# Optimization experiments

Hardware: AMD Instinct MI355X
Metric: run time of the kernel (lower is better)

## Reference

```python
import jax, jax.numpy as jnp
import numpy as np
from jax import lax

B, N = 8, 4096
H = 128          # cfg.net.num_hidden
K = 64           # max_num_neighbors
R1, R2 = 0.2, 0.4
S1, S2 = N // 2, N // 8   # sampling ratios 0.5 and 0.25
OUT = 40


def setup_inputs() -> dict:
    key = jax.random.key(0)
    ks = jax.random.split(key, 32)
    inp = {}
    inp["x"] = jax.random.normal(ks[30], (B, N, 3), jnp.float32)
    inp["pos"] = jax.random.uniform(ks[31], (B, N, 3), jnp.float32)  # unit cube -> radii 0.2/0.4 meaningful
    layers = [("sa1_w1", "sa1_b1", 6, H // 2), ("sa1_w2", "sa1_b2", H // 2, H),
              ("sa2_w1", "sa2_b1", H + 3, H), ("sa2_w2", "sa2_b2", H, 2 * H),
              ("sa3_w1", "sa3_b1", 2 * H + 3, 2 * H), ("sa3_w2", "sa3_b2", 2 * H, 4 * H),
              ("sa3_w3", "sa3_b3", 4 * H, 8 * H),
              ("hd_w1", "hd_b1", 8 * H, 4 * H), ("hd_w2", "hd_b2", 4 * H, 2 * H),
              ("hd_w3", "hd_b3", 2 * H, OUT)]
    for i, (wn, bn, fi, fo) in enumerate(layers):
        inp[wn] = jax.random.normal(ks[i], (fi, fo), jnp.float32) / np.sqrt(fi)
        inp[bn] = jnp.zeros((fo,), jnp.float32)
    return inp


def _mlp(h, layers):
    # Linear+ReLU stack, plain last layer (PyG MLP plain_last=True, eval-mode BN is identity)
    n = len(layers)
    for i, (w, b) in enumerate(layers):
        h = h @ w + b
        if i < n - 1:
            h = jax.nn.relu(h)
    return h


def _fps(p, n_samples):
    # farthest point sampling on one cloud p: [N,3] -> [n_samples] int32
    Np = p.shape[0]

    def step(carry, _):
        min_d, last = carry
        d = jnp.sum((p - p[last]) ** 2, -1)
        min_d = jnp.minimum(min_d, d)
        return (min_d, jnp.argmax(min_d).astype(jnp.int32)), last

    _, idxs = lax.scan(step, (jnp.full((Np,), jnp.inf, p.dtype), jnp.int32(0)),
                       None, length=n_samples)
    return idxs


def _sa(xc, pc, n_samples, r, layers):
    # one SA layer on one cloud: xc [N,C], pc [N,3]
    idx = _fps(pc, n_samples)
    c = pc[idx]                                            # [S,3] centers
    d2 = jnp.sum((c[:, None, :] - pc[None, :, :]) ** 2, -1)  # [S,N]
    d2 = jnp.where(d2 <= r * r, d2, jnp.inf)               # ball query mask
    negd, nbr = lax.top_k(-d2, K)                          # K nearest inside ball
    valid = jnp.isfinite(negd)                             # [S,K]
    feat = jnp.concatenate([xc[nbr], pc[nbr] - c[:, None, :]], -1)  # [S,K,C+3]
    h = _mlp(feat, layers)                                 # [S,K,Cout]
    h = jnp.where(valid[..., None], h, -jnp.inf)
    return jnp.max(h, axis=1), c                           # max-pool over neighborhood


def reference(x, pos, sa1_w1, sa1_b1, sa1_w2, sa1_b2,
              sa2_w1, sa2_b1, sa2_w2, sa2_b2,
              sa3_w1, sa3_b1, sa3_w2, sa3_b2, sa3_w3, sa3_b3,
              hd_w1, hd_b1, hd_w2, hd_b2, hd_w3, hd_b3):
    x1, p1 = jax.vmap(lambda xc, pc: _sa(xc, pc, S1, R1,
                                         [(sa1_w1, sa1_b1), (sa1_w2, sa1_b2)]))(x, pos)
    x2, p2 = jax.vmap(lambda xc, pc: _sa(xc, pc, S2, R2,
                                         [(sa2_w1, sa2_b1), (sa2_w2, sa2_b2)]))(x1, p1)
    # GlobalSAModule: MLP(cat([x,pos])) then global max pool over remaining points
    g = _mlp(jnp.concatenate([x2, p2], -1),
             [(sa3_w1, sa3_b1), (sa3_w2, sa3_b2), (sa3_w3, sa3_b3)])
    g = jnp.max(g, axis=1)                                 # [B, 8H]
    # head MLP (dropout inactive at eval)
    return _mlp(g, [(hd_w1, hd_b1), (hd_w2, hd_b2), (hd_w3, hd_b3)])
```

## Files before the change

kernel.cpp:

```cpp
#include <hip/hip_runtime.h>


constexpr int NBATCH = 8;

template<int CTRL>
__device__ __forceinline__ float dpp_max_step(float v) {
  int o = __builtin_amdgcn_update_dpp(__float_as_int(v), __float_as_int(v),
                                      CTRL, 0xf, 0xf, false);
  return fmaxf(v, __int_as_float(o));
}
__device__ __forceinline__ float wave_max_bcast(float v) {
  v = dpp_max_step<0x111>(v);
  v = dpp_max_step<0x112>(v);
  v = dpp_max_step<0x114>(v);
  v = dpp_max_step<0x118>(v);
  v = dpp_max_step<0x142>(v);
  v = dpp_max_step<0x143>(v);
  return __int_as_float(__builtin_amdgcn_readlane(__float_as_int(v), 63));
}
template<int CTRL>
__device__ __forceinline__ int dpp_add_step(int v) {
  int o = __builtin_amdgcn_update_dpp(0, v, CTRL, 0xf, 0xf, true);
  return v + o;
}
__device__ __forceinline__ int wave_sum_bcast(int v) {
  v = dpp_add_step<0x111>(v);
  v = dpp_add_step<0x112>(v);
  v = dpp_add_step<0x114>(v);
  v = dpp_add_step<0x118>(v);
  v = dpp_add_step<0x142>(v);
  v = dpp_add_step<0x143>(v);
  return __builtin_amdgcn_readlane(v, 63);
}

template<int NPTS, int NTH, int NSAMP>
__device__ void fps_body(const float* __restrict__ p, float* __restrict__ cb) {
#pragma clang fp contract(off)
  constexpr int PT = NPTS / NTH;
  constexpr int NW = NTH / 64;
  __shared__ float lx[NPTS], ly[NPTS], lz[NPTS];
  __shared__ unsigned long long wkey[2][NW];
  __shared__ int sidx[NSAMP];
  const int t = threadIdx.x, lane = t & 63, w = t >> 6;
  float px[PT], py[PT], pz[PT], md[PT];
#pragma unroll
  for (int i = 0; i < PT; i++) {
    int j = t * PT + i;
    px[i] = p[j * 3 + 0]; py[i] = p[j * 3 + 1]; pz[i] = p[j * 3 + 2];
    lx[j] = px[i]; ly[j] = py[i]; lz[j] = pz[i];
    md[i] = __builtin_inff();
  }
  __syncthreads();
  int cur = 0;
  for (int s = 0;; ++s) {
    float cx = lx[cur], cy = ly[cur], cz = lz[cur];
    if (t == 0) sidx[s] = cur;
    if (s == NSAMP - 1) break;
    float bv = -__builtin_inff(); int bi = 0;
#pragma unroll
    for (int i = 0; i < PT; i++) {
      float dx = px[i] - cx, dy = py[i] - cy, dz = pz[i] - cz;
      float d = (dx * dx + dy * dy) + dz * dz;
      float m = fminf(md[i], d); md[i] = m;
      if (m > bv) { bv = m; bi = i; }
    }
    float wmax = wave_max_bcast(bv);
    unsigned long long ball = __ballot(bv == wmax);
    int fl = __ffsll((long long)ball) - 1;
    int ib = __builtin_amdgcn_readlane(bi, fl);
    int gidx = ((w << 6) + fl) * PT + ib;
    if (lane == 0)
      wkey[s & 1][w] = (((unsigned long long)(unsigned)__float_as_int(wmax)) << 32)
                       | (unsigned)(~gidx);
    __syncthreads();
    unsigned long long best = wkey[s & 1][0];
#pragma unroll
    for (int q = 1; q < NW; q++) {
      unsigned long long k2 = wkey[s & 1][q];
      if (k2 > best) best = k2;
    }
    cur = (int)(~(unsigned)best);
  }
  __syncthreads();
  for (int i = t; i < NSAMP; i += NTH) {
    int id = sidx[i];
    cb[i * 3 + 0] = lx[id]; cb[i * 3 + 1] = ly[id]; cb[i * 3 + 2] = lz[id];
  }
}

template<int NPTS, int SPB>
__device__ void ballquery_body(int bb, const float* __restrict__ pts,
    const float* __restrict__ ctr, float rr,
    int* __restrict__ nbr, int* __restrict__ cnt_out) {
#pragma clang fp contract(off)
  const int gw = (bb << 2) + (threadIdx.x >> 6);
  const int lane = threadIdx.x & 63;
  const int b = gw / SPB;
  __shared__ unsigned long long list_[4][1024];
  unsigned long long* list = list_[threadIdx.x >> 6];
  const float* p = pts + (size_t)b * NPTS * 3;
  const float* c = ctr + (size_t)gw * 3;
  const float cx = c[0], cy = c[1], cz = c[2];
  const unsigned long long lmask = (1ull << lane) - 1ull;
  int cnt = 0;
  for (int j0 = 0; j0 < NPTS; j0 += 64) {
    int j = j0 + lane;
    float dx = p[j * 3 + 0] - cx, dy = p[j * 3 + 1] - cy, dz = p[j * 3 + 2] - cz;
    float d = (dx * dx + dy * dy) + dz * dz;
    bool in = (d <= rr);
    unsigned long long bal = __ballot(in);
    int pos = cnt + __popcll(bal & lmask);
    if (in && pos < 1024)
      list[pos] = (((unsigned long long)__float_as_uint(d)) << 32) | (unsigned)j;
    cnt += __popcll(bal);
  }
  if (cnt > 1024) cnt = 1024;
  __syncthreads();
  int* nbrp = nbr + (size_t)gw * 64;
  const int nr = (cnt + 63) >> 6;
  unsigned long long key[16];
#pragma unroll
  for (int r = 0; r < 16; r++) {
    int slot = r * 64 + lane;
    key[r] = (r < nr && slot < cnt) ? list[slot] : ~0ull;
  }
  if (cnt <= 64) {
    nbrp[lane] = (lane < cnt) ? (int)(unsigned)key[0] : 0;
    if (lane == 0) cnt_out[gw] = cnt;
    return;
  }
  unsigned pref = 0; int cbase = 0;
  for (int bit = 29; bit >= 0; --bit) {
    int cc = 0;
#pragma unroll
    for (int r = 0; r < 16; r++) if (r < nr) {
      unsigned db = (unsigned)(key[r] >> 32);
      cc += ((db >> bit) == (pref >> bit)) ? 1 : 0;
    }
    cc = wave_sum_bcast(cc);
    if (cbase + cc < 64) { cbase += cc; pref |= (1u << bit); }
  }
  int base = 0;
#pragma unroll
  for (int r = 0; r < 16; r++) if (r < nr) {
    unsigned db = (unsigned)(key[r] >> 32);
    bool sel = db < pref;
    unsigned long long m = __ballot(sel);
    if (sel) nbrp[base + __popcll(m & lmask)] = (int)(unsigned)key[r];
    base += __popcll(m);
  }
  int need = 64 - base;
  for (int t2 = 0; t2 < need; ++t2) {
    unsigned besti = 0xffffffffu;
#pragma unroll
    for (int r = 0; r < 16; r++) if (r < nr) {
      if ((unsigned)(key[r] >> 32) == pref) {
        unsigned v = (unsigned)key[r];
        besti = v < besti ? v : besti;
      }
    }
#pragma unroll
    for (int off = 32; off; off >>= 1) {
      unsigned o = __shfl_xor(besti, off, 64);
      besti = o < besti ? o : besti;
    }
    unsigned long long wk = (((unsigned long long)pref) << 32) | besti;
#pragma unroll
    for (int r = 0; r < 16; r++) if (r < nr && key[r] == wk) key[r] = ~0ull;
    if (lane == 0) nbrp[base + t2] = (int)besti;
  }
  if (lane == 0) cnt_out[gw] = 64;
}

__device__ void q1_body(int bb, const float* __restrict__ x,
    const float* __restrict__ pos, const float* __restrict__ w, float* __restrict__ q) {
  int gw = bb * 8 + (threadIdx.x >> 6), lane = threadIdx.x & 63;
  const float* xr = x + (size_t)gw * 3; const float* pr = pos + (size_t)gw * 3;
  float a = 0.f;
#pragma unroll
  for (int m = 0; m < 3; m++) a = fmaf(xr[m], w[m * 64 + lane], a);
#pragma unroll
  for (int m = 0; m < 3; m++) a = fmaf(pr[m], w[(3 + m) * 64 + lane], a);
  q[(size_t)gw * 64 + lane] = a;
}

__device__ void t1_body(int bb, const float* __restrict__ c1,
    const float* __restrict__ w, const float* __restrict__ b1, float* __restrict__ t) {
  int gw = (bb << 2) + (threadIdx.x >> 6), lane = threadIdx.x & 63;
  const float* cr = c1 + (size_t)gw * 3;
  float a = b1[lane];
#pragma unroll
  for (int m = 0; m < 3; m++) a = fmaf(-cr[m], w[(3 + m) * 64 + lane], a);
  t[(size_t)gw * 64 + lane] = a;
}

__device__ void t2_body(int bb, const float* __restrict__ c2,
    const float* __restrict__ w, const float* __restrict__ b1, float* __restrict__ t) {
  int gw = (bb << 2) + (threadIdx.x >> 6), lane = threadIdx.x & 63;
  const float* cr = c2 + (size_t)gw * 3;
  float a0 = b1[lane], a1 = b1[64 + lane];
#pragma unroll
  for (int m = 0; m < 3; m++) {
    a0 = fmaf(-cr[m], w[(128 + m) * 128 + lane], a0);
    a1 = fmaf(-cr[m], w[(128 + m) * 128 + 64 + lane], a1);
  }
  t[(size_t)gw * 128 + lane] = a0;
  t[(size_t)gw * 128 + 64 + lane] = a1;
}

__device__ void concat3_body(int bb, const float* __restrict__ c2, float* __restrict__ xin3) {
  int row = bb * 256 + threadIdx.x;
  if (row < NBATCH * 512) {
    float* o = xin3 + (size_t)row * 272 + 256;
    const float* c = c2 + (size_t)row * 3;
    o[0] = c[0]; o[1] = c[1]; o[2] = c[2];
#pragma unroll
    for (int i = 3; i < 16; i++) o[i] = 0.f;
  }
}

template<int CIN, int COUT, int OSTR, int NPB, int SPB>
__device__ void sa_pool_body(int bb, const float* __restrict__ q,
    const float* __restrict__ t, const int* __restrict__ nbr, const int* __restrict__ cnt,
    const float* __restrict__ w2, const float* __restrict__ b2, float* __restrict__ out) {
  int gw = (bb << 2) + (threadIdx.x >> 6), lane = threadIdx.x & 63;
  int b = gw / SPB;
  int nk = nbr[(size_t)gw * 64 + lane];
  int c = cnt[gw];
  const float* qr = q + ((size_t)b * NPB + nk) * CIN;
  const float* tr = t + (size_t)gw * CIN;
  float h[CIN];
#pragma unroll
  for (int i = 0; i < CIN; i += 4) {
    float4 v = *(const float4*)(qr + i);
    h[i]     = fmaxf(v.x + tr[i], 0.f);
    h[i + 1] = fmaxf(v.y + tr[i + 1], 0.f);
    h[i + 2] = fmaxf(v.z + tr[i + 2], 0.f);
    h[i + 3] = fmaxf(v.w + tr[i + 3], 0.f);
  }
  bool valid = lane < c;
  float* op = out + (size_t)gw * OSTR;
#pragma unroll 1
  for (int nc = 0; nc < COUT; nc += 16) {
    float acc[16];
#pragma unroll
    for (int u = 0; u < 16; u++) acc[u] = b2[nc + u];
#pragma unroll
    for (int i = 0; i < CIN; i++) {
      const float* wr = w2 + (size_t)i * COUT + nc;
#pragma unroll
      for (int u = 0; u < 16; u++) acc[u] = fmaf(h[i], wr[u], acc[u]);
    }
#pragma unroll
    for (int u = 0; u < 16; u++) {
      float v = valid ? acc[u] : -__builtin_inff();
#pragma unroll
      for (int off = 32; off; off >>= 1) v = fmaxf(v, __shfl_xor(v, off, 64));
      acc[u] = v;
    }
    if (lane == 0) {
#pragma unroll
      for (int u = 0; u < 16; u += 4)
        *(float4*)(op + nc + u) = make_float4(acc[u], acc[u + 1], acc[u + 2], acc[u + 3]);
    }
  }
}

__global__ __launch_bounds__(512) void fuse1_kernel(const float* __restrict__ pos,
    const float* __restrict__ x, const float* __restrict__ w11,
    float* __restrict__ c1, float* __restrict__ q1) {
  int bid = blockIdx.x;
  if (bid < 8)
    fps_body<4096, 512, 2048>(pos + (size_t)bid * 4096 * 3, c1 + (size_t)bid * 2048 * 3);
  else
    q1_body(bid - 8, x, pos, w11, q1);
}

__global__ __launch_bounds__(256) void fuse2_kernel(const float* __restrict__ pos,
    const float* __restrict__ c1, const float* __restrict__ w11, const float* __restrict__ b11,
    float* __restrict__ c2, int* __restrict__ nbr1, int* __restrict__ cnt1,
    float* __restrict__ t1buf, float rr1) {
  int bid = blockIdx.x;
  if (bid < 8)
    fps_body<2048, 256, 512>(c1 + (size_t)bid * 2048 * 3, c2 + (size_t)bid * 512 * 3);
  else if (bid < 8 + 4096)
    ballquery_body<4096, 2048>(bid - 8, pos, c1, rr1, nbr1, cnt1);
  else
    t1_body(bid - (8 + 4096), c1, w11, b11, t1buf);
}

__global__ __launch_bounds__(256) void fuse3_kernel(const float* __restrict__ q1buf,
    const float* __restrict__ t1buf, const int* __restrict__ nbr1, const int* __restrict__ cnt1,
    const float* __restrict__ w12, const float* __restrict__ b12, float* __restrict__ x1,
    const float* __restrict__ c1, const float* __restrict__ c2, float rr2,
    int* __restrict__ nbr2, int* __restrict__ cnt2,
    const float* __restrict__ w21, const float* __restrict__ b21, float* __restrict__ t2buf,
    float* __restrict__ xin3) {
  int bid = blockIdx.x;
  if (bid < 4096)
    sa_pool_body<64, 128, 128, 4096, 2048>(bid, q1buf, t1buf, nbr1, cnt1, w12, b12, x1);
  else if (bid < 4096 + 1024)
    ballquery_body<2048, 512>(bid - 4096, c1, c2, rr2, nbr2, cnt2);
  else if (bid < 4096 + 1024 + 1024)
    t2_body(bid - (4096 + 1024), c2, w21, b21, t2buf);
  else
    concat3_body(bid - (4096 + 1024 + 1024), c2, xin3);
}

__global__ __launch_bounds__(256) void q2_kernel(const float* __restrict__ x1,
    const float* __restrict__ p1, const float* __restrict__ w, float* __restrict__ q2) {
  int gw = (blockIdx.x << 2) + (threadIdx.x >> 6), lane = threadIdx.x & 63;
  const float* xr = x1 + (size_t)gw * 128; const float* pr = p1 + (size_t)gw * 3;
  float a0 = 0.f, a1 = 0.f;
#pragma unroll 8
  for (int m = 0; m < 128; m++) {
    float v = xr[m];
    a0 = fmaf(v, w[m * 128 + lane], a0);
    a1 = fmaf(v, w[m * 128 + 64 + lane], a1);
  }
#pragma unroll
  for (int m = 0; m < 3; m++) {
    float v = pr[m];
    a0 = fmaf(v, w[(128 + m) * 128 + lane], a0);
    a1 = fmaf(v, w[(128 + m) * 128 + 64 + lane], a1);
  }
  q2[(size_t)gw * 128 + lane] = a0;
  q2[(size_t)gw * 128 + 64 + lane] = a1;
}

__global__ __launch_bounds__(256) void sa_pool2_kernel(const float* __restrict__ q,
    const float* __restrict__ t, const int* __restrict__ nbr, const int* __restrict__ cnt,
    const float* __restrict__ w2, const float* __restrict__ b2, float* __restrict__ out) {
  sa_pool_body<128, 256, 272, 2048, 512>(blockIdx.x, q, t, nbr, cnt, w2, b2, out);
}

template<int K, int KP, int N, int AST, bool RELU>
__global__ __launch_bounds__(256) void gemm64(const float* __restrict__ A,
    const float* __restrict__ W, const float* __restrict__ bias, float* __restrict__ C) {
  constexpr int NT = N / 64;
  const int bid = blockIdx.x, tid = threadIdx.x;
  const int tm = bid / NT, tn = bid % NT;
  __shared__ __align__(16) float As[16][68];
  __shared__ __align__(16) float Ws[16][68];
  const int arow = tid >> 2, acol = (tid & 3) << 2;
  const int wrow = tid >> 4, wcol = (tid & 15) << 2;
  const int ty = tid >> 4, tx = tid & 15;
  const float* Ap = A + (size_t)(tm * 64 + arow) * AST + acol;
  const float* Wp = W + (size_t)tn * 64 + wcol;
  float acc[4][4] = {};
  for (int k0 = 0; k0 < KP; k0 += 16) {
    float4 av = *(const float4*)(Ap + k0);
    As[acol + 0][arow] = av.x; As[acol + 1][arow] = av.y;
    As[acol + 2][arow] = av.z; As[acol + 3][arow] = av.w;
    int krow = k0 + wrow;
    float4 wv = make_float4(0.f, 0.f, 0.f, 0.f);
    if (krow < K) wv = *(const float4*)(Wp + (size_t)krow * N);
    *(float4*)(&Ws[wrow][wcol]) = wv;
    __syncthreads();
#pragma unroll
    for (int kk = 0; kk < 16; kk++) {
      float4 a4 = *(const float4*)(&As[kk][ty << 2]);
      float4 b4 = *(const float4*)(&Ws[kk][tx << 2]);
      float aa[4] = {a4.x, a4.y, a4.z, a4.w};
      float bb[4] = {b4.x, b4.y, b4.z, b4.w};
#pragma unroll
      for (int mm = 0; mm < 4; mm++)
#pragma unroll
        for (int nn = 0; nn < 4; nn++) acc[mm][nn] = fmaf(aa[mm], bb[nn], acc[mm][nn]);
    }
    __syncthreads();
  }
  const int m0 = tm * 64 + (ty << 2), n0 = tn * 64 + (tx << 2);
#pragma unroll
  for (int mm = 0; mm < 4; mm++) {
    float4 o;
    o.x = acc[mm][0] + bias[n0 + 0];
    o.y = acc[mm][1] + bias[n0 + 1];
    o.z = acc[mm][2] + bias[n0 + 2];
    o.w = acc[mm][3] + bias[n0 + 3];
    if (RELU) { o.x = fmaxf(o.x, 0.f); o.y = fmaxf(o.y, 0.f);
                o.z = fmaxf(o.z, 0.f); o.w = fmaxf(o.w, 0.f); }
    *(float4*)(C + (size_t)(m0 + mm) * N + n0) = o;
  }
}

__global__ void gmax_kernel(const float* __restrict__ h, float* __restrict__ g) {
  int n = blockIdx.x * 256 + threadIdx.x;
  int b = n >> 10, col = n & 1023;
  const float* p = h + ((size_t)b * 512) * 1024 + col;
  float m = -__builtin_inff();
  for (int j = 0; j < 512; j++) m = fmaxf(m, p[(size_t)j * 1024]);
  g[n] = m;
}

__global__ __launch_bounds__(256) void head_kernel(const float* __restrict__ g,
    const float* __restrict__ w1, const float* __restrict__ b1,
    const float* __restrict__ w2, const float* __restrict__ b2,
    const float* __restrict__ w3, const float* __restrict__ b3,
    float* __restrict__ out) {
  int b = blockIdx.x, t = threadIdx.x;
  __shared__ float s1[1024];
  __shared__ float s2[512];
  *(float4*)(s1 + t * 4) = *(const float4*)(g + (size_t)b * 1024 + t * 4);
  __syncthreads();
  {
    float a0 = b1[t], a1 = b1[t + 256];
    for (int i = 0; i < 1024; i++) {
      float v = s1[i];
      a0 = fmaf(v, w1[(size_t)i * 512 + t], a0);
      a1 = fmaf(v, w1[(size_t)i * 512 + t + 256], a1);
    }
    s2[t] = fmaxf(a0, 0.f); s2[t + 256] = fmaxf(a1, 0.f);
  }
  __syncthreads();
  {
    float a = b2[t];
    for (int i = 0; i < 512; i++) a = fmaf(s2[i], w2[(size_t)i * 256 + t], a);
    s1[t] = fmaxf(a, 0.f);
  }
  __syncthreads();
  if (t < 40) {
    float a = b3[t];
    for (int i = 0; i < 256; i++) a = fmaf(s1[i], w3[(size_t)i * 40 + t], a);
    out[(size_t)b * 40 + t] = a;
  }
}

extern "C" void kernel_launch(void* const* d_in, const int* in_sizes, int n_in,
                              void* d_out, int out_size, void* d_ws, size_t ws_size,
                              hipStream_t stream) {
  const float* x   = (const float*)d_in[0];
  const float* pos = (const float*)d_in[1];
  const float* w11 = (const float*)d_in[2];  const float* b11 = (const float*)d_in[3];
  const float* w12 = (const float*)d_in[4];  const float* b12 = (const float*)d_in[5];
  const float* w21 = (const float*)d_in[6];  const float* b21 = (const float*)d_in[7];
  const float* w22 = (const float*)d_in[8];  const float* b22 = (const float*)d_in[9];
  const float* w31 = (const float*)d_in[10]; const float* b31 = (const float*)d_in[11];
  const float* w32 = (const float*)d_in[12]; const float* b32 = (const float*)d_in[13];
  const float* w33 = (const float*)d_in[14]; const float* b33 = (const float*)d_in[15];
  const float* hw1 = (const float*)d_in[16]; const float* hb1 = (const float*)d_in[17];
  const float* hw2 = (const float*)d_in[18]; const float* hb2 = (const float*)d_in[19];
  const float* hw3 = (const float*)d_in[20]; const float* hb3 = (const float*)d_in[21];
  float* out = (float*)d_out;

  char* wsb = (char*)d_ws;
  int*   cnt1 = (int*)(wsb + 81920);
  int*   cnt2 = (int*)(wsb + 147456);
  float* c1   = (float*)(wsb + 163840);
  float* c2   = (float*)(wsb + 360448);
  float* g    = (float*)(wsb + 409600);
  char* big = wsb + 524288;
  int*   nbr1 = (int*)(big + 0);
  float* q1   = (float*)(big + 4194304);
  float* t1   = (float*)(big + 12582912);
  float* h3c  = (float*)(big + 0);
  float* x1   = (float*)(big + 16777216);
  int*   nbr2 = (int*)(big + 25165824);
  float* h3b  = (float*)(big + 16777216);
  float* q2   = (float*)(big + 26214400);
  float* h3a  = (float*)(big + 26214400);
  float* t2   = (float*)(big + 34603008);
  float* xin3 = (float*)(big + 36700160);

  const float RR1 = (float)(0.2 * 0.2);
  const float RR2 = (float)(0.4 * 0.4);

  fuse1_kernel<<<8 + 4096, 512, 0, stream>>>(pos, x, w11, c1, q1);
  fuse2_kernel<<<8 + 4096 + 4096, 256, 0, stream>>>(pos, c1, w11, b11,
                                                    c2, nbr1, cnt1, t1, RR1);
  fuse3_kernel<<<4096 + 1024 + 1024 + 16, 256, 0, stream>>>(q1, t1, nbr1, cnt1,
      w12, b12, x1, c1, c2, RR2, nbr2, cnt2, w21, b21, t2, xin3);
  q2_kernel<<<4096, 256, 0, stream>>>(x1, c1, w21, q2);
  sa_pool2_kernel<<<1024, 256, 0, stream>>>(q2, t2, nbr2, cnt2, w22, b22, xin3);
  gemm64<259, 272, 256, 272, true ><<<256,  256, 0, stream>>>(xin3, w31, b31, h3a);
  gemm64<256, 256, 512, 256, true ><<<512,  256, 0, stream>>>(h3a,  w32, b32, h3b);
  gemm64<512, 512, 1024, 512, false><<<1024, 256, 0, stream>>>(h3b, w33, b33, h3c);
  gmax_kernel<<<32, 256, 0, stream>>>(h3c, g);
  head_kernel<<<NBATCH, 256, 0, stream>>>(g, hw1, hb1, hw2, hb2, hw3, hb3, out);

  (void)in_sizes; (void)n_in; (void)out_size; (void)ws_size;
}
```

Measured before the change: 3.535 ms.

## Interleave four clouds per FPS block with packed math and register-carried centers

Result: slower. 8.536 ms (+141.5%).

```diff
diff --git a/kernel.cpp b/kernel.cpp
--- a/kernel.cpp
+++ b/kernel.cpp
@@ -2,6 +2,8 @@
 
 
 constexpr int NBATCH = 8;
+
+typedef float v2f __attribute__((ext_vector_type(2)));
 
 template<int CTRL>
 __device__ __forceinline__ float dpp_max_step(float v) {
@@ -33,70 +35,215 @@
   return __builtin_amdgcn_readlane(v, 63);
 }
 
-template<int NPTS, int NTH, int NSAMP>
-__device__ void fps_body(const float* __restrict__ p, float* __restrict__ cb) {
+#define DIST_PAIR(PX, PY, PZ, MD) { \
+  v2f dx = PX - cxv; v2f dy = PY - cyv; v2f dz = PZ - czv; \
+  v2f d = (dx * dx + dy * dy) + dz * dz; \
+  MD = __builtin_elementwise_min(MD, d); \
+  bv2 = __builtin_elementwise_max(bv2, MD); }
+
+__device__ void fps1_quad(const float* __restrict__ pos4, float* __restrict__ cb4) {
 #pragma clang fp contract(off)
-  constexpr int PT = NPTS / NTH;
-  constexpr int NW = NTH / 64;
-  __shared__ float lx[NPTS], ly[NPTS], lz[NPTS];
-  __shared__ unsigned long long wkey[2][NW];
-  __shared__ int sidx[NSAMP];
+  constexpr int NPTS = 4096, NTH = 512, PT = 8, NW = 8, NSAMP = 2048;
+  __shared__ unsigned long long skey[2][4][NW];
+  __shared__ float sxyz[2][4][NW][3];
+  __shared__ float scb[4][NSAMP * 3];
   const int t = threadIdx.x, lane = t & 63, w = t >> 6;
-  float px[PT], py[PT], pz[PT], md[PT];
-#pragma unroll
-  for (int i = 0; i < PT; i++) {
-    int j = t * PT + i;
-    px[i] = p[j * 3 + 0]; py[i] = p[j * 3 + 1]; pz[i] = p[j * 3 + 2];
-    lx[j] = px[i]; ly[j] = py[i]; lz[j] = pz[i];
-    md[i] = __builtin_inff();
+  const float INF = __builtin_inff();
+
+#define F1_REGS(B) \
+  v2f px0_##B, px1_##B, px2_##B, px3_##B; \
+  v2f py0_##B, py1_##B, py2_##B, py3_##B; \
+  v2f pz0_##B, pz1_##B, pz2_##B, pz3_##B; \
+  v2f md0_##B, md1_##B, md2_##B, md3_##B; \
+  float cx_##B, cy_##B, cz_##B;
+  F1_REGS(0) F1_REGS(1) F1_REGS(2) F1_REGS(3)
+
+#define F1_LOAD(B) { \
+  const float* pp = pos4 + (size_t)(B) * NPTS * 3; \
+  int jb = t * PT; \
+  px0_##B = (v2f){pp[(jb+0)*3+0], pp[(jb+1)*3+0]}; \
+  py0_##B = (v2f){pp[(jb+0)*3+1], pp[(jb+1)*3+1]}; \
+  pz0_##B = (v2f){pp[(jb+0)*3+2], pp[(jb+1)*3+2]}; \
+  px1_##B = (v2f){pp[(jb+2)*3+0], pp[(jb+3)*3+0]}; \
+  py1_##B = (v2f){pp[(jb+2)*3+1], pp[(jb+3)*3+1]}; \
+  pz1_##B = (v2f){pp[(jb+2)*3+2], pp[(jb+3)*3+2]}; \
+  px2_##B = (v2f){pp[(jb+4)*3+0], pp[(jb+5)*3+0]}; \
+  py2_##B = (v2f){pp[(jb+4)*3+1], pp[(jb+5)*3+1]}; \
+  pz2_##B = (v2f){pp[(jb+4)*3+2], pp[(jb+5)*3+2]}; \
+  px3_##B = (v2f){pp[(jb+6)*3+0], pp[(jb+7)*3+0]}; \
+  py3_##B = (v2f){pp[(jb+6)*3+1], pp[(jb+7)*3+1]}; \
+  pz3_##B = (v2f){pp[(jb+6)*3+2], pp[(jb+7)*3+2]}; \
+  md0_##B = (v2f){INF, INF}; md1_##B = (v2f){INF, INF}; \
+  md2_##B = (v2f){INF, INF}; md3_##B = (v2f){INF, INF}; \
+  cx_##B = pp[0]; cy_##B = pp[1]; cz_##B = pp[2]; \
+  if (t == 0) { scb[B][0] = cx_##B; scb[B][1] = cy_##B; scb[B][2] = cz_##B; } }
+  F1_LOAD(0) F1_LOAD(1) F1_LOAD(2) F1_LOAD(3)
+
+#define F1_PHASEA(B) { \
+  v2f cxv = {cx_##B, cx_##B}, cyv = {cy_##B, cy_##B}, czv = {cz_##B, cz_##B}; \
+  v2f bv2 = (v2f){-INF, -INF}; \
+  DIST_PAIR(px0_##B, py0_##B, pz0_##B, md0_##B) \
+  DIST_PAIR(px1_##B, py1_##B, pz1_##B, md1_##B) \
+  DIST_PAIR(px2_##B, py2_##B, pz2_##B, md2_##B) \
+  DIST_PAIR(px3_##B, py3_##B, pz3_##B, md3_##B) \
+  float bv = fmaxf(bv2.x, bv2.y); \
+  int bi = 0; \
+  if (md3_##B.y == bv) bi = 7; \
+  if (md3_##B.x == bv) bi = 6; \
+  if (md2_##B.y == bv) bi = 5; \
+  if (md2_##B.x == bv) bi = 4; \
+  if (md1_##B.y == bv) bi = 3; \
+  if (md1_##B.x == bv) bi = 2; \
+  if (md0_##B.y == bv) bi = 1; \
+  if (md0_##B.x == bv) bi = 0; \
+  float wmax = wave_max_bcast(bv); \
+  unsigned long long ball = __ballot(bv == wmax); \
+  int fl = __ffsll((long long)ball) - 1; \
+  int ib = __builtin_amdgcn_readlane(bi, fl); \
+  int gidx = ((w << 6) + fl) * PT + ib; \
+  int kk = ib >> 1; \
+  v2f sx = px0_##B, sy = py0_##B, sz = pz0_##B; \
+  if (kk == 1) { sx = px1_##B; sy = py1_##B; sz = pz1_##B; } \
+  if (kk == 2) { sx = px2_##B; sy = py2_##B; sz = pz2_##B; } \
+  if (kk == 3) { sx = px3_##B; sy = py3_##B; sz = pz3_##B; } \
+  float wx = (ib & 1) ? sx.y : sx.x; \
+  float wy = (ib & 1) ? sy.y : sy.x; \
+  float wz = (ib & 1) ? sz.y : sz.x; \
+  wx = __int_as_float(__builtin_amdgcn_readlane(__float_as_int(wx), fl)); \
+  wy = __int_as_float(__builtin_amdgcn_readlane(__float_as_int(wy), fl)); \
+  wz = __int_as_float(__builtin_amdgcn_readlane(__float_as_int(wz), fl)); \
+  if (lane == 0) { \
+    skey[s & 1][B][w] = (((unsigned long long)(unsigned)__float_as_int(wmax)) << 32) \
+                        | (unsigned)(~gidx); \
+    sxyz[s & 1][B][w][0] = wx; sxyz[s & 1][B][w][1] = wy; sxyz[s & 1][B][w][2] = wz; } }
+
+#define F1_PHASEB(B) { \
+  unsigned long long best = skey[s & 1][B][0]; int qw = 0; \
+  _Pragma("unroll") \
+  for (int q = 1; q < NW; q++) { \
+    unsigned long long k2 = skey[s & 1][B][q]; \
+    if (k2 > best) { best = k2; qw = q; } } \
+  cx_##B = sxyz[s & 1][B][qw][0]; \
+  cy_##B = sxyz[s & 1][B][qw][1]; \
+  cz_##B = sxyz[s & 1][B][qw][2]; \
+  if (t == 0) { scb[B][(s + 1) * 3 + 0] = cx_##B; \
+                scb[B][(s + 1) * 3 + 1] = cy_##B; \
+                scb[B][(s + 1) * 3 + 2] = cz_##B; } }
+
+  for (int s = 0; s < NSAMP - 1; ++s) {
+    F1_PHASEA(0) F1_PHASEA(1) F1_PHASEA(2) F1_PHASEA(3)
+    __syncthreads();
+    F1_PHASEB(0) F1_PHASEB(1) F1_PHASEB(2) F1_PHASEB(3)
   }
   __syncthreads();
-  int cur = 0;
-  for (int s = 0;; ++s) {
-    float cx = lx[cur], cy = ly[cur], cz = lz[cur];
-    if (t == 0) sidx[s] = cur;
-    if (s == NSAMP - 1) break;
-    float bv = -__builtin_inff(); int bi = 0;
-#pragma unroll
-    for (int i = 0; i < PT; i++) {
-      float dx = px[i] - cx, dy = py[i] - cy, dz = pz[i] - cz;
-      float d = (dx * dx + dy * dy) + dz * dz;
-      float m = fminf(md[i], d); md[i] = m;
-      if (m > bv) { bv = m; bi = i; }
-    }
-    float wmax = wave_max_bcast(bv);
-    unsigned long long ball = __ballot(bv == wmax);
-    int fl = __ffsll((long long)ball) - 1;
-    int ib = __builtin_amdgcn_readlane(bi, fl);
-    int gidx = ((w << 6) + fl) * PT + ib;
-    if (lane == 0)
-      wkey[s & 1][w] = (((unsigned long long)(unsigned)__float_as_int(wmax)) << 32)
-                       | (unsigned)(~gidx);
+#pragma unroll
+  for (int B = 0; B < 4; B++)
+    for (int i = t; i < NSAMP * 3; i += NTH)
+      cb4[(size_t)B * NSAMP * 3 + i] = scb[B][i];
+#undef F1_REGS
+#undef F1_LOAD
+#undef F1_PHASEA
+#undef F1_PHASEB
+}
+
+__device__ void fps2_quad(const float* __restrict__ pos4, float* __restrict__ cb4) {
+#pragma clang fp contract(off)
+  constexpr int NPTS = 2048, NTH = 512, PT = 4, NW = 8, NSAMP = 512;
+  __shared__ unsigned long long skey2[2][4][NW];
+  __shared__ float sxyz2[2][4][NW][3];
+  __shared__ float scb2[4][NSAMP * 3];
+  const int t = threadIdx.x, lane = t & 63, w = t >> 6;
+  const float INF = __builtin_inff();
+
+#define F2_REGS(B) \
+  v2f px0_##B, px1_##B, py0_##B, py1_##B, pz0_##B, pz1_##B; \
+  v2f md0_##B, md1_##B; \
+  float cx_##B, cy_##B, cz_##B;
+  F2_REGS(0) F2_REGS(1) F2_REGS(2) F2_REGS(3)
+
+#define F2_LOAD(B) { \
+  const float* pp = pos4 + (size_t)(B) * NPTS * 3; \
+  int jb = t * PT; \
+  px0_##B = (v2f){pp[(jb+0)*3+0], pp[(jb+1)*3+0]}; \
+  py0_##B = (v2f){pp[(jb+0)*3+1], pp[(jb+1)*3+1]}; \
+  pz0_##B = (v2f){pp[(jb+0)*3+2], pp[(jb+1)*3+2]}; \
+  px1_##B = (v2f){pp[(jb+2)*3+0], pp[(jb+3)*3+0]}; \
+  py1_##B = (v2f){pp[(jb+2)*3+1], pp[(jb+3)*3+1]}; \
+  pz1_##B = (v2f){pp[(jb+2)*3+2], pp[(jb+3)*3+2]}; \
+  md0_##B = (v2f){INF, INF}; md1_##B = (v2f){INF, INF}; \
+  cx_##B = pp[0]; cy_##B = pp[1]; cz_##B = pp[2]; \
+  if (t == 0) { scb2[B][0] = cx_##B; scb2[B][1] = cy_##B; scb2[B][2] = cz_##B; } }
+  F2_LOAD(0) F2_LOAD(1) F2_LOAD(2) F2_LOAD(3)
+
+#define F2_PHASEA(B) { \
+  v2f cxv = {cx_##B, cx_##B}, cyv = {cy_##B, cy_##B}, czv = {cz_##B, cz_##B}; \
+  v2f bv2 = (v2f){-INF, -INF}; \
+  DIST_PAIR(px0_##B, py0_##B, pz0_##B, md0_##B) \
+  DIST_PAIR(px1_##B, py1_##B, pz1_##B, md1_##B) \
+  float bv = fmaxf(bv2.x, bv2.y); \
+  int bi = 0; \
+  if (md1_##B.y == bv) bi = 3; \
+  if (md1_##B.x == bv) bi = 2; \
+  if (md0_##B.y == bv) bi = 1; \
+  if (md0_##B.x == bv) bi = 0; \
+  float wmax = wave_max_bcast(bv); \
+  unsigned long long ball = __ballot(bv == wmax); \
+  int fl = __ffsll((long long)ball) - 1; \
+  int ib = __builtin_amdgcn_readlane(bi, fl); \
+  int gidx = ((w << 6) + fl) * PT + ib; \
+  int kk = ib >> 1; \
+  v2f sx = px0_##B, sy = py0_##B, sz = pz0_##B; \
+  if (kk == 1) { sx = px1_##B; sy = py1_##B; sz = pz1_##B; } \
+  float wx = (ib & 1) ? sx.y : sx.x; \
+  float wy = (ib & 1) ? sy.y : sy.x; \
+  float wz = (ib & 1) ? sz.y : sz.x; \
+  wx = __int_as_float(__builtin_amdgcn_readlane(__float_as_int(wx), fl)); \
+  wy = __int_as_float(__builtin_amdgcn_readlane(__float_as_int(wy), fl)); \
+  wz = __int_as_float(__builtin_amdgcn_readlane(__float_as_int(wz), fl)); \
+  if (lane == 0) { \
+    skey2[s & 1][B][w] = (((unsigned long long)(unsigned)__float_as_int(wmax)) << 32) \
+                         | (unsigned)(~gidx); \
+    sxyz2[s & 1][B][w][0] = wx; sxyz2[s & 1][B][w][1] = wy; sxyz2[s & 1][B][w][2] = wz; } }
+
+#define F2_PHASEB(B) { \
+  unsigned long long best = skey2[s & 1][B][0]; int qw = 0; \
+  _Pragma("unroll") \
+  for (int q = 1; q < NW; q++) { \
+    unsigned long long k2 = skey2[s & 1][B][q]; \
+    if (k2 > best) { best = k2; qw = q; } } \
+  cx_##B = sxyz2[s & 1][B][qw][0]; \
+  cy_##B = sxyz2[s & 1][B][qw][1]; \
+  cz_##B = sxyz2[s & 1][B][qw][2]; \
+  if (t == 0) { scb2[B][(s + 1) * 3 + 0] = cx_##B; \
+                scb2[B][(s + 1) * 3 + 1] = cy_##B; \
+                scb2[B][(s + 1) * 3 + 2] = cz_##B; } }
+
+  for (int s = 0; s < NSAMP - 1; ++s) {
+    F2_PHASEA(0) F2_PHASEA(1) F2_PHASEA(2) F2_PHASEA(3)
     __syncthreads();
-    unsigned long long best = wkey[s & 1][0];
-#pragma unroll
-    for (int q = 1; q < NW; q++) {
-      unsigned long long k2 = wkey[s & 1][q];
-      if (k2 > best) best = k2;
-    }
-    cur = (int)(~(unsigned)best);
+    F2_PHASEB(0) F2_PHASEB(1) F2_PHASEB(2) F2_PHASEB(3)
   }
   __syncthreads();
-  for (int i = t; i < NSAMP; i += NTH) {
-    int id = sidx[i];
-    cb[i * 3 + 0] = lx[id]; cb[i * 3 + 1] = ly[id]; cb[i * 3 + 2] = lz[id];
-  }
-}
-
-template<int NPTS, int SPB>
+#pragma unroll
+  for (int B = 0; B < 4; B++)
+    for (int i = t; i < NSAMP * 3; i += NTH)
+      cb4[(size_t)B * NSAMP * 3 + i] = scb2[B][i];
+#undef F2_REGS
+#undef F2_LOAD
+#undef F2_PHASEA
+#undef F2_PHASEB
+}
+
+template<int NPTS, int SPB, int LCAP, int WPB>
 __device__ void ballquery_body(int bb, const float* __restrict__ pts,
     const float* __restrict__ ctr, float rr,
     int* __restrict__ nbr, int* __restrict__ cnt_out) {
 #pragma clang fp contract(off)
-  const int gw = (bb << 2) + (threadIdx.x >> 6);
+  constexpr int KREG = LCAP / 64;
+  const int gw = bb * WPB + (threadIdx.x >> 6);
   const int lane = threadIdx.x & 63;
   const int b = gw / SPB;
-  __shared__ unsigned long long list_[4][1024];
+  __shared__ unsigned long long list_[WPB][LCAP];
   unsigned long long* list = list_[threadIdx.x >> 6];
   const float* p = pts + (size_t)b * NPTS * 3;
   const float* c = ctr + (size_t)gw * 3;
@@ -110,17 +257,17 @@
     bool in = (d <= rr);
     unsigned long long bal = __ballot(in);
     int pos = cnt + __popcll(bal & lmask);
-    if (in && pos < 1024)
+    if (in && pos < LCAP)
       list[pos] = (((unsigned long long)__float_as_uint(d)) << 32) | (unsigned)j;
     cnt += __popcll(bal);
   }
-  if (cnt > 1024) cnt = 1024;
+  if (cnt > LCAP) cnt = LCAP;
   __syncthreads();
   int* nbrp = nbr + (size_t)gw * 64;
   const int nr = (cnt + 63) >> 6;
-  unsigned long long key[16];
-#pragma unroll
-  for (int r = 0; r < 16; r++) {
+  unsigned long long key[KREG];
+#pragma unroll
+  for (int r = 0; r < KREG; r++) {
     int slot = r * 64 + lane;
     key[r] = (r < nr && slot < cnt) ? list[slot] : ~0ull;
   }
@@ -133,7 +280,7 @@
   for (int bit = 29; bit >= 0; --bit) {
     int cc = 0;
 #pragma unroll
-    for (int r = 0; r < 16; r++) if (r < nr) {
+    for (int r = 0; r < KREG; r++) if (r < nr) {
       unsigned db = (unsigned)(key[r] >> 32);
       cc += ((db >> bit) == (pref >> bit)) ? 1 : 0;
     }
@@ -142,7 +289,7 @@
   }
   int base = 0;
 #pragma unroll
-  for (int r = 0; r < 16; r++) if (r < nr) {
+  for (int r = 0; r < KREG; r++) if (r < nr) {
     unsigned db = (unsigned)(key[r] >> 32);
     bool sel = db < pref;
     unsigned long long m = __ballot(sel);
@@ -153,7 +300,7 @@
   for (int t2 = 0; t2 < need; ++t2) {
     unsigned besti = 0xffffffffu;
 #pragma unroll
-    for (int r = 0; r < 16; r++) if (r < nr) {
+    for (int r = 0; r < KREG; r++) if (r < nr) {
       if ((unsigned)(key[r] >> 32) == pref) {
         unsigned v = (unsigned)key[r];
         besti = v < besti ? v : besti;
@@ -166,7 +313,7 @@
     }
     unsigned long long wk = (((unsigned long long)pref) << 32) | besti;
 #pragma unroll
-    for (int r = 0; r < 16; r++) if (r < nr && key[r] == wk) key[r] = ~0ull;
+    for (int r = 0; r < KREG; r++) if (r < nr && key[r] == wk) key[r] = ~0ull;
     if (lane == 0) nbrp[base + t2] = (int)besti;
   }
   if (lane == 0) cnt_out[gw] = 64;
@@ -186,7 +333,7 @@
 
 __device__ void t1_body(int bb, const float* __restrict__ c1,
     const float* __restrict__ w, const float* __restrict__ b1, float* __restrict__ t) {
-  int gw = (bb << 2) + (threadIdx.x >> 6), lane = threadIdx.x & 63;
+  int gw = bb * 8 + (threadIdx.x >> 6), lane = threadIdx.x & 63;
   const float* cr = c1 + (size_t)gw * 3;
   float a = b1[lane];
 #pragma unroll
@@ -270,23 +417,23 @@
     const float* __restrict__ x, const float* __restrict__ w11,
     float* __restrict__ c1, float* __restrict__ q1) {
   int bid = blockIdx.x;
-  if (bid < 8)
-    fps_body<4096, 512, 2048>(pos + (size_t)bid * 4096 * 3, c1 + (size_t)bid * 2048 * 3);
+  if (bid < 2)
+    fps1_quad(pos + (size_t)bid * 4 * 4096 * 3, c1 + (size_t)bid * 4 * 2048 * 3);
   else
-    q1_body(bid - 8, x, pos, w11, q1);
-}
-
-__global__ __launch_bounds__(256) void fuse2_kernel(const float* __restrict__ pos,
+    q1_body(bid - 2, x, pos, w11, q1);
+}
+
+__global__ __launch_bounds__(512) void fuse2_kernel(const float* __restrict__ pos,
     const float* __restrict__ c1, const float* __restrict__ w11, const float* __restrict__ b11,
     float* __restrict__ c2, int* __restrict__ nbr1, int* __restrict__ cnt1,
     float* __restrict__ t1buf, float rr1) {
   int bid = blockIdx.x;
-  if (bid < 8)
-    fps_body<2048, 256, 512>(c1 + (size_t)bid * 2048 * 3, c2 + (size_t)bid * 512 * 3);
-  else if (bid < 8 + 4096)
-    ballquery_body<4096, 2048>(bid - 8, pos, c1, rr1, nbr1, cnt1);
+  if (bid < 2)
+    fps2_quad(c1 + (size_t)bid * 4 * 2048 * 3, c2 + (size_t)bid * 4 * 512 * 3);
+  else if (bid < 2 + 2048)
+    ballquery_body<4096, 2048, 512, 8>(bid - 2, pos, c1, rr1, nbr1, cnt1);
   else
-    t1_body(bid - (8 + 4096), c1, w11, b11, t1buf);
+    t1_body(bid - (2 + 2048), c1, w11, b11, t1buf);
 }
 
 __global__ __launch_bounds__(256) void fuse3_kernel(const float* __restrict__ q1buf,
@@ -300,7 +447,7 @@
   if (bid < 4096)
     sa_pool_body<64, 128, 128, 4096, 2048>(bid, q1buf, t1buf, nbr1, cnt1, w12, b12, x1);
   else if (bid < 4096 + 1024)
-    ballquery_body<2048, 512>(bid - 4096, c1, c2, rr2, nbr2, cnt2);
+    ballquery_body<2048, 512, 1024, 4>(bid - 4096, c1, c2, rr2, nbr2, cnt2);
   else if (bid < 4096 + 1024 + 1024)
     t2_body(bid - (4096 + 1024), c2, w21, b21, t2buf);
   else
@@ -465,8 +612,8 @@
   const float RR1 = (float)(0.2 * 0.2);
   const float RR2 = (float)(0.4 * 0.4);
 
-  fuse1_kernel<<<8 + 4096, 512, 0, stream>>>(pos, x, w11, c1, q1);
-  fuse2_kernel<<<8 + 4096 + 4096, 256, 0, stream>>>(pos, c1, w11, b11,
+  fuse1_kernel<<<2 + 4096, 512, 0, stream>>>(pos, x, w11, c1, q1);
+  fuse2_kernel<<<2 + 2048 + 2048, 512, 0, stream>>>(pos, c1, w11, b11,
                                                     c2, nbr1, cnt1, t1, RR1);
   fuse3_kernel<<<4096 + 1024 + 1024 + 16, 256, 0, stream>>>(q1, t1, nbr1, cnt1,
       w12, b12, x1, c1, c2, RR2, nbr2, cnt2, w21, b21, t2, xin3);
```

## Vectorize FPS with packed float2 math and carry winner coordinates through reduction

Applied to the files above, without the earlier changes.

Measured after the change: 4.116 ms. 1.16x slower.

```diff
diff --git a/kernel.cpp b/kernel.cpp
--- a/kernel.cpp
+++ b/kernel.cpp
@@ -2,6 +2,8 @@
 
 
 constexpr int NBATCH = 8;
+
+typedef float v2f __attribute__((ext_vector_type(2)));
 
 template<int CTRL>
 __device__ __forceinline__ float dpp_max_step(float v) {
@@ -33,70 +35,180 @@
   return __builtin_amdgcn_readlane(v, 63);
 }
 
-template<int NPTS, int NTH, int NSAMP>
-__device__ void fps_body(const float* __restrict__ p, float* __restrict__ cb) {
+#define DIST_PAIR(PX, PY, PZ, MD) { \
+  v2f dx = PX - cxv; v2f dy = PY - cyv; v2f dz = PZ - czv; \
+  v2f d = (dx * dx + dy * dy) + dz * dz; \
+  MD = __builtin_elementwise_min(MD, d); \
+  bv2 = __builtin_elementwise_max(bv2, MD); }
+
+__device__ void fps1_one(const float* __restrict__ p, float* __restrict__ cb) {
 #pragma clang fp contract(off)
-  constexpr int PT = NPTS / NTH;
-  constexpr int NW = NTH / 64;
-  __shared__ float lx[NPTS], ly[NPTS], lz[NPTS];
-  __shared__ unsigned long long wkey[2][NW];
-  __shared__ int sidx[NSAMP];
+  constexpr int NTH = 512, PT = 8, NW = 8, NSAMP = 2048;
+  __shared__ unsigned long long skey[2][NW];
+  __shared__ float sxyz[2][NW][3];
+  __shared__ float scb[NSAMP * 3];
   const int t = threadIdx.x, lane = t & 63, w = t >> 6;
-  float px[PT], py[PT], pz[PT], md[PT];
-#pragma unroll
-  for (int i = 0; i < PT; i++) {
-    int j = t * PT + i;
-    px[i] = p[j * 3 + 0]; py[i] = p[j * 3 + 1]; pz[i] = p[j * 3 + 2];
-    lx[j] = px[i]; ly[j] = py[i]; lz[j] = pz[i];
-    md[i] = __builtin_inff();
-  }
-  __syncthreads();
-  int cur = 0;
-  for (int s = 0;; ++s) {
-    float cx = lx[cur], cy = ly[cur], cz = lz[cur];
-    if (t == 0) sidx[s] = cur;
-    if (s == NSAMP - 1) break;
-    float bv = -__builtin_inff(); int bi = 0;
-#pragma unroll
-    for (int i = 0; i < PT; i++) {
-      float dx = px[i] - cx, dy = py[i] - cy, dz = pz[i] - cz;
-      float d = (dx * dx + dy * dy) + dz * dz;
-      float m = fminf(md[i], d); md[i] = m;
-      if (m > bv) { bv = m; bi = i; }
-    }
+  const float INF = __builtin_inff();
+  v2f px0, px1, px2, px3, py0, py1, py2, py3, pz0, pz1, pz2, pz3;
+  v2f md0, md1, md2, md3;
+  {
+    int jb = t * PT;
+    px0 = (v2f){p[(jb+0)*3+0], p[(jb+1)*3+0]};
+    py0 = (v2f){p[(jb+0)*3+1], p[(jb+1)*3+1]};
+    pz0 = (v2f){p[(jb+0)*3+2], p[(jb+1)*3+2]};
+    px1 = (v2f){p[(jb+2)*3+0], p[(jb+3)*3+0]};
+    py1 = (v2f){p[(jb+2)*3+1], p[(jb+3)*3+1]};
+    pz1 = (v2f){p[(jb+2)*3+2], p[(jb+3)*3+2]};
+    px2 = (v2f){p[(jb+4)*3+0], p[(jb+5)*3+0]};
+    py2 = (v2f){p[(jb+4)*3+1], p[(jb+5)*3+1]};
+    pz2 = (v2f){p[(jb+4)*3+2], p[(jb+5)*3+2]};
+    px3 = (v2f){p[(jb+6)*3+0], p[(jb+7)*3+0]};
+    py3 = (v2f){p[(jb+6)*3+1], p[(jb+7)*3+1]};
+    pz3 = (v2f){p[(jb+6)*3+2], p[(jb+7)*3+2]};
+    md0 = (v2f){INF, INF}; md1 = (v2f){INF, INF};
+    md2 = (v2f){INF, INF}; md3 = (v2f){INF, INF};
+  }
+  float cx = p[0], cy = p[1], cz = p[2];
+  if (t == 0) { scb[0] = cx; scb[1] = cy; scb[2] = cz; }
+  for (int s = 0; s < NSAMP - 1; ++s) {
+    v2f cxv = {cx, cx}, cyv = {cy, cy}, czv = {cz, cz};
+    v2f bv2 = (v2f){-INF, -INF};
+    DIST_PAIR(px0, py0, pz0, md0)
+    DIST_PAIR(px1, py1, pz1, md1)
+    DIST_PAIR(px2, py2, pz2, md2)
+    DIST_PAIR(px3, py3, pz3, md3)
+    float bv = fmaxf(bv2.x, bv2.y);
+    int bi = 0;
+    if (md3.y == bv) bi = 7;
+    if (md3.x == bv) bi = 6;
+    if (md2.y == bv) bi = 5;
+    if (md2.x == bv) bi = 4;
+    if (md1.y == bv) bi = 3;
+    if (md1.x == bv) bi = 2;
+    if (md0.y == bv) bi = 1;
+    if (md0.x == bv) bi = 0;
     float wmax = wave_max_bcast(bv);
     unsigned long long ball = __ballot(bv == wmax);
     int fl = __ffsll((long long)ball) - 1;
     int ib = __builtin_amdgcn_readlane(bi, fl);
     int gidx = ((w << 6) + fl) * PT + ib;
-    if (lane == 0)
-      wkey[s & 1][w] = (((unsigned long long)(unsigned)__float_as_int(wmax)) << 32)
+    int kk = ib >> 1;
+    v2f sx = px0, sy = py0, sz = pz0;
+    if (kk == 1) { sx = px1; sy = py1; sz = pz1; }
+    if (kk == 2) { sx = px2; sy = py2; sz = pz2; }
+    if (kk == 3) { sx = px3; sy = py3; sz = pz3; }
+    float wx = (ib & 1) ? sx.y : sx.x;
+    float wy = (ib & 1) ? sy.y : sy.x;
+    float wz = (ib & 1) ? sz.y : sz.x;
+    wx = __int_as_float(__builtin_amdgcn_readlane(__float_as_int(wx), fl));
+    wy = __int_as_float(__builtin_amdgcn_readlane(__float_as_int(wy), fl));
+    wz = __int_as_float(__builtin_amdgcn_readlane(__float_as_int(wz), fl));
+    if (lane == 0) {
+      skey[s & 1][w] = (((unsigned long long)(unsigned)__float_as_int(wmax)) << 32)
                        | (unsigned)(~gidx);
+      sxyz[s & 1][w][0] = wx; sxyz[s & 1][w][1] = wy; sxyz[s & 1][w][2] = wz;
+    }
     __syncthreads();
-    unsigned long long best = wkey[s & 1][0];
+    unsigned long long best = skey[s & 1][0];
+    float nx = sxyz[s & 1][0][0], ny = sxyz[s & 1][0][1], nz = sxyz[s & 1][0][2];
 #pragma unroll
     for (int q = 1; q < NW; q++) {
-      unsigned long long k2 = wkey[s & 1][q];
-      if (k2 > best) best = k2;
-    }
-    cur = (int)(~(unsigned)best);
+      unsigned long long k2 = skey[s & 1][q];
+      bool gt = k2 > best;
+      best = gt ? k2 : best;
+      nx = gt ? sxyz[s & 1][q][0] : nx;
+      ny = gt ? sxyz[s & 1][q][1] : ny;
+      nz = gt ? sxyz[s & 1][q][2] : nz;
+    }
+    cx = nx; cy = ny; cz = nz;
+    if (t == 0) { scb[(s + 1) * 3 + 0] = cx; scb[(s + 1) * 3 + 1] = cy;
+                  scb[(s + 1) * 3 + 2] = cz; }
   }
   __syncthreads();
-  for (int i = t; i < NSAMP; i += NTH) {
-    int id = sidx[i];
-    cb[i * 3 + 0] = lx[id]; cb[i * 3 + 1] = ly[id]; cb[i * 3 + 2] = lz[id];
-  }
-}
-
-template<int NPTS, int SPB>
+  for (int i = t; i < NSAMP * 3; i += NTH) cb[i] = scb[i];
+}
+
+__device__ void fps2_one(const float* __restrict__ p, float* __restrict__ cb) {
+#pragma clang fp contract(off)
+  constexpr int NTH = 512, PT = 4, NW = 8, NSAMP = 512;
+  __shared__ unsigned long long skey2[2][NW];
+  __shared__ float sxyz2[2][NW][3];
+  __shared__ float scb2[NSAMP * 3];
+  const int t = threadIdx.x, lane = t & 63, w = t >> 6;
+  const float INF = __builtin_inff();
+  v2f px0, px1, py0, py1, pz0, pz1, md0, md1;
+  {
+    int jb = t * PT;
+    px0 = (v2f){p[(jb+0)*3+0], p[(jb+1)*3+0]};
+    py0 = (v2f){p[(jb+0)*3+1], p[(jb+1)*3+1]};
+    pz0 = (v2f){p[(jb+0)*3+2], p[(jb+1)*3+2]};
+    px1 = (v2f){p[(jb+2)*3+0], p[(jb+3)*3+0]};
+    py1 = (v2f){p[(jb+2)*3+1], p[(jb+3)*3+1]};
+    pz1 = (v2f){p[(jb+2)*3+2], p[(jb+3)*3+2]};
+    md0 = (v2f){INF, INF}; md1 = (v2f){INF, INF};
+  }
+  float cx = p[0], cy = p[1], cz = p[2];
+  if (t == 0) { scb2[0] = cx; scb2[1] = cy; scb2[2] = cz; }
+  for (int s = 0; s < NSAMP - 1; ++s) {
+    v2f cxv = {cx, cx}, cyv = {cy, cy}, czv = {cz, cz};
+    v2f bv2 = (v2f){-INF, -INF};
+    DIST_PAIR(px0, py0, pz0, md0)
+    DIST_PAIR(px1, py1, pz1, md1)
+    float bv = fmaxf(bv2.x, bv2.y);
+    int bi = 0;
+    if (md1.y == bv) bi = 3;
+    if (md1.x == bv) bi = 2;
+    if (md0.y == bv) bi = 1;
+    if (md0.x == bv) bi = 0;
+    float wmax = wave_max_bcast(bv);
+    unsigned long long ball = __ballot(bv == wmax);
+    int fl = __ffsll((long long)ball) - 1;
+    int ib = __builtin_amdgcn_readlane(bi, fl);
+    int gidx = ((w << 6) + fl) * PT + ib;
+    int kk = ib >> 1;
+    v2f sx = px0, sy = py0, sz = pz0;
+    if (kk == 1) { sx = px1; sy = py1; sz = pz1; }
+    float wx = (ib & 1) ? sx.y : sx.x;
+    float wy = (ib & 1) ? sy.y : sy.x;
+    float wz = (ib & 1) ? sz.y : sz.x;
+    wx = __int_as_float(__builtin_amdgcn_readlane(__float_as_int(wx), fl));
+    wy = __int_as_float(__builtin_amdgcn_readlane(__float_as_int(wy), fl));
+    wz = __int_as_float(__builtin_amdgcn_readlane(__float_as_int(wz), fl));
+    if (lane == 0) {
+      skey2[s & 1][w] = (((unsigned long long)(unsigned)__float_as_int(wmax)) << 32)
+                        | (unsigned)(~gidx);
+      sxyz2[s & 1][w][0] = wx; sxyz2[s & 1][w][1] = wy; sxyz2[s & 1][w][2] = wz;
+    }
+    __syncthreads();
+    unsigned long long best = skey2[s & 1][0];
+    float nx = sxyz2[s & 1][0][0], ny = sxyz2[s & 1][0][1], nz = sxyz2[s & 1][0][2];
+#pragma unroll
+    for (int q = 1; q < NW; q++) {
+      unsigned long long k2 = skey2[s & 1][q];
+      bool gt = k2 > best;
+      best = gt ? k2 : best;
+      nx = gt ? sxyz2[s & 1][q][0] : nx;
+      ny = gt ? sxyz2[s & 1][q][1] : ny;
+      nz = gt ? sxyz2[s & 1][q][2] : nz;
+    }
+    cx = nx; cy = ny; cz = nz;
+    if (t == 0) { scb2[(s + 1) * 3 + 0] = cx; scb2[(s + 1) * 3 + 1] = cy;
+                  scb2[(s + 1) * 3 + 2] = cz; }
+  }
+  __syncthreads();
+  for (int i = t; i < NSAMP * 3; i += NTH) cb[i] = scb2[i];
+}
+
+template<int NPTS, int SPB, int LCAP, int WPB>
 __device__ void ballquery_body(int bb, const float* __restrict__ pts,
     const float* __restrict__ ctr, float rr,
     int* __restrict__ nbr, int* __restrict__ cnt_out) {
 #pragma clang fp contract(off)
-  const int gw = (bb << 2) + (threadIdx.x >> 6);
+  constexpr int KREG = LCAP / 64;
+  const int gw = bb * WPB + (threadIdx.x >> 6);
   const int lane = threadIdx.x & 63;
   const int b = gw / SPB;
-  __shared__ unsigned long long list_[4][1024];
+  __shared__ unsigned long long list_[WPB][LCAP];
   unsigned long long* list = list_[threadIdx.x >> 6];
   const float* p = pts + (size_t)b * NPTS * 3;
   const float* c = ctr + (size_t)gw * 3;
@@ -110,17 +222,17 @@
     bool in = (d <= rr);
     unsigned long long bal = __ballot(in);
     int pos = cnt + __popcll(bal & lmask);
-    if (in && pos < 1024)
+    if (in && pos < LCAP)
       list[pos] = (((unsigned long long)__float_as_uint(d)) << 32) | (unsigned)j;
     cnt += __popcll(bal);
   }
-  if (cnt > 1024) cnt = 1024;
+  if (cnt > LCAP) cnt = LCAP;
   __syncthreads();
   int* nbrp = nbr + (size_t)gw * 64;
   const int nr = (cnt + 63) >> 6;
-  unsigned long long key[16];
-#pragma unroll
-  for (int r = 0; r < 16; r++) {
+  unsigned long long key[KREG];
+#pragma unroll
+  for (int r = 0; r < KREG; r++) {
     int slot = r * 64 + lane;
     key[r] = (r < nr && slot < cnt) ? list[slot] : ~0ull;
   }
@@ -133,7 +245,7 @@
   for (int bit = 29; bit >= 0; --bit) {
     int cc = 0;
 #pragma unroll
-    for (int r = 0; r < 16; r++) if (r < nr) {
+    for (int r = 0; r < KREG; r++) if (r < nr) {
       unsigned db = (unsigned)(key[r] >> 32);
       cc += ((db >> bit) == (pref >> bit)) ? 1 : 0;
     }
@@ -142,7 +254,7 @@
   }
   int base = 0;
 #pragma unroll
-  for (int r = 0; r < 16; r++) if (r < nr) {
+  for (int r = 0; r < KREG; r++) if (r < nr) {
     unsigned db = (unsigned)(key[r] >> 32);
     bool sel = db < pref;
     unsigned long long m = __ballot(sel);
@@ -153,7 +265,7 @@
   for (int t2 = 0; t2 < need; ++t2) {
     unsigned besti = 0xffffffffu;
 #pragma unroll
-    for (int r = 0; r < 16; r++) if (r < nr) {
+    for (int r = 0; r < KREG; r++) if (r < nr) {
       if ((unsigned)(key[r] >> 32) == pref) {
         unsigned v = (unsigned)key[r];
         besti = v < besti ? v : besti;
@@ -166,7 +278,7 @@
     }
     unsigned long long wk = (((unsigned long long)pref) << 32) | besti;
 #pragma unroll
-    for (int r = 0; r < 16; r++) if (r < nr && key[r] == wk) key[r] = ~0ull;
+    for (int r = 0; r < KREG; r++) if (r < nr && key[r] == wk) key[r] = ~0ull;
     if (lane == 0) nbrp[base + t2] = (int)besti;
   }
   if (lane == 0) cnt_out[gw] = 64;
@@ -186,7 +298,7 @@
 
 __device__ void t1_body(int bb, const float* __restrict__ c1,
     const float* __restrict__ w, const float* __restrict__ b1, float* __restrict__ t) {
-  int gw = (bb << 2) + (threadIdx.x >> 6), lane = threadIdx.x & 63;
+  int gw = bb * 8 + (threadIdx.x >> 6), lane = threadIdx.x & 63;
   const float* cr = c1 + (size_t)gw * 3;
   float a = b1[lane];
 #pragma unroll
@@ -266,27 +378,27 @@
   }
 }
 
-__global__ __launch_bounds__(512) void fuse1_kernel(const float* __restrict__ pos,
+__global__ __launch_bounds__(512, 2) void fuse1_kernel(const float* __restrict__ pos,
     const float* __restrict__ x, const float* __restrict__ w11,
     float* __restrict__ c1, float* __restrict__ q1) {
   int bid = blockIdx.x;
   if (bid < 8)
-    fps_body<4096, 512, 2048>(pos + (size_t)bid * 4096 * 3, c1 + (size_t)bid * 2048 * 3);
+    fps1_one(pos + (size_t)bid * 4096 * 3, c1 + (size_t)bid * 2048 * 3);
   else
     q1_body(bid - 8, x, pos, w11, q1);
 }
 
-__global__ __launch_bounds__(256) void fuse2_kernel(const float* __restrict__ pos,
+__global__ __launch_bounds__(512, 2) void fuse2_kernel(const float* __restrict__ pos,
     const float* __restrict__ c1, const float* __restrict__ w11, const float* __restrict__ b11,
     float* __restrict__ c2, int* __restrict__ nbr1, int* __restrict__ cnt1,
     float* __restrict__ t1buf, float rr1) {
   int bid = blockIdx.x;
   if (bid < 8)
-    fps_body<2048, 256, 512>(c1 + (size_t)bid * 2048 * 3, c2 + (size_t)bid * 512 * 3);
-  else if (bid < 8 + 4096)
-    ballquery_body<4096, 2048>(bid - 8, pos, c1, rr1, nbr1, cnt1);
+    fps2_one(c1 + (size_t)bid * 2048 * 3, c2 + (size_t)bid * 512 * 3);
+  else if (bid < 8 + 2048)
+    ballquery_body<4096, 2048, 512, 8>(bid - 8, pos, c1, rr1, nbr1, cnt1);
   else
-    t1_body(bid - (8 + 4096), c1, w11, b11, t1buf);
+    t1_body(bid - (8 + 2048), c1, w11, b11, t1buf);
 }
 
 __global__ __launch_bounds__(256) void fuse3_kernel(const float* __restrict__ q1buf,
@@ -300,7 +412,7 @@
   if (bid < 4096)
     sa_pool_body<64, 128, 128, 4096, 2048>(bid, q1buf, t1buf, nbr1, cnt1, w12, b12, x1);
   else if (bid < 4096 + 1024)
-    ballquery_body<2048, 512>(bid - 4096, c1, c2, rr2, nbr2, cnt2);
+    ballquery_body<2048, 512, 1024, 4>(bid - 4096, c1, c2, rr2, nbr2, cnt2);
   else if (bid < 4096 + 1024 + 1024)
     t2_body(bid - (4096 + 1024), c2, w21, b21, t2buf);
   else
@@ -466,7 +578,7 @@
   const float RR2 = (float)(0.4 * 0.4);
 
   fuse1_kernel<<<8 + 4096, 512, 0, stream>>>(pos, x, w11, c1, q1);
-  fuse2_kernel<<<8 + 4096 + 4096, 256, 0, stream>>>(pos, c1, w11, b11,
+  fuse2_kernel<<<8 + 2048 + 2048, 512, 0, stream>>>(pos, c1, w11, b11,
                                                     c2, nbr1, cnt1, t1, RR1);
   fuse3_kernel<<<4096 + 1024 + 1024 + 16, 256, 0, stream>>>(q1, t1, nbr1, cnt1,
       w12, b12, x1, c1, c2, RR2, nbr2, cnt2, w21, b21, t2, xin3);
```
